# Kernel optimization log

Measured on AMD Instinct MI355X. Metric: run time of the kernel, lower is better.

## Reference

```python
import jax, jax.numpy as jnp
import numpy as np

N = 4096  # number of nodes (matches fill_max of edge indices)


def _dense(edges, n):
    # edges: [2, E] int; dense {0,1} adjacency. Duplicate edges collapse (set semantics).
    return jnp.zeros((n, n), dtype=jnp.float32).at[edges[0], edges[1]].set(1.0)


def setup_inputs() -> dict:
    key = jax.random.key(0)
    ks = jax.random.split(key, 4)
    E = 200000
    mk = lambda k: jax.random.randint(k, (2, E), 0, N, dtype=jnp.int32)
    return {
        "A_pos_t": mk(ks[0]),
        "A_pos_tp1": mk(ks[1]),
        "A_neg_t": mk(ks[2]),
        "A_neg_tp1": mk(ks[3]),
    }


def reference(A_pos_t, A_pos_tp1, A_neg_t, A_neg_tp1):
    p_t = _dense(A_pos_t, N)
    p1 = _dense(A_pos_tp1, N)
    n_t = _dense(A_neg_t, N)
    n1 = _dense(A_neg_tp1, N)

    # edge_index_diff: set symmetric difference == elementwise xor of {0,1} adjacency
    xor_p = p_t + p1 - 2.0 * p_t * p1
    xor_n = n_t + n1 - 2.0 * n_t * n1

    # Balance theory triangle closure on (tp1) graphs.
    # sign(a,b): +1 if pos edge (pos checked first -> priority), -1 elif neg edge.
    sp = p1                      # positive-sign edge indicator
    sn = n1 * (1.0 - p1)         # negative-sign edge indicator (pos has priority)
    off = 1.0 - jnp.eye(N, dtype=jnp.float32)
    spo = sp * off               # exclude b==a / b==c (triples are distinct)
    sno = sn * off

    # number of 2-paths a->b->c with predicted sign +1 / -1
    M_same = spo @ spo + sno @ sno
    M_diff = spo @ sno + sno @ spo

    # the Python loop only infers edges (a,c) with a < c (orientations (i,j,k),(i,k,j),(j,i,k))
    tri = jnp.triu(jnp.ones((N, N), dtype=jnp.float32), k=1)

    ind_p = M_same * tri * (1.0 - p1)  # skip pairs already positively connected
    ind_n = M_diff * tri * (1.0 - n1)  # skip pairs already negatively connected

    # Output: [2, N, N]; entry = xor indicator + indirect-edge multiplicity count
    return jnp.stack([xor_p + ind_p, xor_n + ind_n])
```

## Files before the change

kernel.cpp:

```cpp
#include <hip/hip_runtime.h>


#define NN 4096
#define NW 128
#define MASK_BYTES ((size_t)NN * NW * 4)
#define MASK_WORDS ((size_t)NN * NW)

typedef unsigned int u32;
typedef __attribute__((ext_vector_type(4))) int int4v;
typedef __attribute__((ext_vector_type(4))) float f32x4;

__device__ __forceinline__ void gload_lds16(const char* g, char* l) {
    __builtin_amdgcn_global_load_lds(
        (const __attribute__((address_space(1))) void*)g,
        (__attribute__((address_space(3))) void*)l, 16, 0, 0);
}


__global__ void scatter_all(const int* __restrict__ e0, const int* __restrict__ e1,
                            const int* __restrict__ e2, const int* __restrict__ e3,
                            int E0, int E1, int E2, int E3,
                            u32* __restrict__ ws) {
    int i = blockIdx.x * blockDim.x + threadIdx.x;
    u32* Pt  = ws + 0 * MASK_WORDS;
    u32* P1  = ws + 1 * MASK_WORDS;
    u32* Nt  = ws + 2 * MASK_WORDS;
    u32* N1  = ws + 3 * MASK_WORDS;
    u32* P1T = ws + 4 * MASK_WORDS;
    u32* N1T = ws + 5 * MASK_WORDS;
    if (i < E0) { int r = e0[i], c = e0[i + E0];
        atomicOr(&Pt[r * NW + (c >> 5)], 1u << (c & 31)); }
    if (i < E1) { int r = e1[i], c = e1[i + E1];
        atomicOr(&P1[r * NW + (c >> 5)], 1u << (c & 31));
        atomicOr(&P1T[c * NW + (r >> 5)], 1u << (r & 31)); }
    if (i < E2) { int r = e2[i], c = e2[i + E2];
        atomicOr(&Nt[r * NW + (c >> 5)], 1u << (c & 31)); }
    if (i < E3) { int r = e3[i], c = e3[i + E3];
        atomicOr(&N1[r * NW + (c >> 5)], 1u << (c & 31));
        atomicOr(&N1T[c * NW + (r >> 5)], 1u << (r & 31)); }
}

__device__ __forceinline__ int4v expand_e(u32 sp, u32 sn) {
    int4v E;
    #pragma unroll
    for (int i = 0; i < 4; i++) {
        u32 p = (((sp >> (4 * i)) & 0xFu) * 0x00204081u) & 0x01010101u;
        u32 n = (((sn >> (4 * i)) & 0xFu) * 0x00204081u) & 0x01010101u;
        E[i] = (int)(p | (n << 5));
    }
    return E;
}

__global__ void build_e(const u32* __restrict__ masks,
                        char* __restrict__ E, char* __restrict__ ET) {
    int u = blockIdx.x * blockDim.x + threadIdx.x;
    int half = (u >= (int)MASK_WORDS);
    int wi = half ? u - (int)MASK_WORDS : u;
    const u32* P  = masks + (half ? 4 : 1) * MASK_WORDS;
    const u32* Nm = masks + (half ? 5 : 3) * MASK_WORDS;
    u32 p = P[wi];
    u32 n = Nm[wi] & ~p;
    int a = wi >> 7, col = wi & 127;
    if ((a >> 5) == col) {
        u32 db = 1u << (a & 31);
        p &= ~db; n &= ~db;
    }
    char* dst = (half ? ET : E) + (size_t)a * NN;
    #pragma unroll
    for (int j = 0; j < 2; j++) {
        int kb = col * 32 + j * 16;
        int kbs = (kb & ~127) | (((((kb >> 4) & 7) ^ (a & 7)) & 7) << 4);
        *reinterpret_cast<int4v*>(dst + kbs) =
            expand_e((p >> (16 * j)) & 0xFFFFu, (n >> (16 * j)) & 0xFFFFu);
    }
}

__global__ __launch_bounds__(256, 2) void gemm_ep(
    const char* __restrict__ E, const char* __restrict__ ET,
    const u32* __restrict__ Pt, const u32* __restrict__ P1,
    const u32* __restrict__ Nt, const u32* __restrict__ N1,
    float* __restrict__ out)
{
    const int tid = threadIdx.x;
    const size_t plane = (size_t)NN * NN;

    int s_ = ((int)blockIdx.x & 7) * 66 + ((int)blockIdx.x >> 3);
    int by = (int)((65.0f - sqrtf(4225.0f - 8.0f * (float)s_)) * 0.5f);
    if (by > 31) by = 31;
    while (by > 0 && 32 * by - (by * (by - 1)) / 2 > s_) --by;
    while (32 * (by + 1) - ((by + 1) * by) / 2 <= s_) ++by;
    int bx = by + s_ - (32 * by - (by * (by - 1)) / 2);
    const int a0 = by << 7, c0 = bx << 7;

    __shared__ char EA[2][16384];
    __shared__ char EB[2][16384];

    const int wave = tid >> 6, lane = tid & 63;
    const int wr = (wave >> 1) * 64, wcol = (wave & 1) * 64;
    const int lr = lane & 15, lg = lane >> 4;

    const char* gA = E  + (size_t)(a0 + (tid >> 3)) * NN + (tid & 7) * 16;
    const char* gB = ET + (size_t)(c0 + (tid >> 3)) * NN + (tid & 7) * 16;
    const int wuni = (tid >> 6) * 1024;

    int4v acc[4][4];
    int4v zero = {0, 0, 0, 0};
    #pragma unroll
    for (int m = 0; m < 4; m++)
        #pragma unroll
        for (int n = 0; n < 4; n++) acc[m][n] = zero;

    #pragma unroll
    for (int i = 0; i < 4; i++) {
        gload_lds16(gA + i * 131072, &EA[0][i * 4096 + wuni]);
        gload_lds16(gB + i * 131072, &EB[0][i * 4096 + wuni]);
    }

    if (by != bx) {
        #pragma unroll 4
        for (int pass = 0; pass < 16; ++pass) {
            int e = pass * 1024 + tid * 4;
            int r = e >> 7, cc = e & 127;
            int widx = (c0 + r) * NW + ((a0 + cc) >> 5);
            int sh = cc & 31;
            u32 xp = (P1[widx] ^ Pt[widx]) >> sh;
            u32 xn = (N1[widx] ^ Nt[widx]) >> sh;
            f32x4 o0, o1;
            #pragma unroll
            for (int i = 0; i < 4; i++) {
                o0[i] = (float)((xp >> i) & 1u);
                o1[i] = (float)((xn >> i) & 1u);
            }
            size_t ob = (size_t)(c0 + r) * NN + a0 + cc;
            *reinterpret_cast<f32x4*>(out + ob) = o0;
            *reinterpret_cast<f32x4*>(out + plane + ob) = o1;
        }
    }
    __syncthreads();

    for (int t = 0; t < 32; ++t) {
        const int cur = t & 1;
        if (t < 31) {
            const int off = (t + 1) * 128;
            #pragma unroll
            for (int i = 0; i < 4; i++) {
                gload_lds16(gA + i * 131072 + off, &EA[cur ^ 1][i * 4096 + wuni]);
                gload_lds16(gB + i * 131072 + off, &EB[cur ^ 1][i * 4096 + wuni]);
            }
        }
        #pragma unroll
        for (int ks = 0; ks < 2; ks++) {
            const int kb = ks * 64 + lg * 16;
            int4v ebf[4];
            #pragma unroll
            for (int n = 0; n < 4; n++) {
                int rowb = wcol + n * 16 + lr;
                ebf[n] = *reinterpret_cast<const int4v*>(
                    &EB[cur][rowb * 128 + (kb ^ ((rowb & 7) << 4))]);
            }
            #pragma unroll
            for (int m = 0; m < 4; m++) {
                int rowa = wr + m * 16 + lr;
                int4v eaf = *reinterpret_cast<const int4v*>(
                    &EA[cur][rowa * 128 + (kb ^ ((rowa & 7) << 4))]);
                #pragma unroll
                for (int n = 0; n < 4; n++)
                    acc[m][n] = __builtin_amdgcn_mfma_i32_16x16x64_i8(
                        eaf, ebf[n], acc[m][n], 0, 0, 0);
            }
        }
        __syncthreads();
    }

    #pragma unroll
    for (int m = 0; m < 4; m++) {
        #pragma unroll
        for (int n = 0; n < 4; n++) {
            #pragma unroll
            for (int q = 0; q < 4; q++) {
                int a = a0 + wr + m * 16 + lg * 4 + q;
                int c = c0 + wcol + n * 16 + lr;
                int widx = a * NW + (c >> 5);
                int bit = c & 31;
                u32 p1 = (P1[widx] >> bit) & 1u;
                u32 n1 = (N1[widx] >> bit) & 1u;
                u32 pt = (Pt[widx] >> bit) & 1u;
                u32 nt = (Nt[widx] >> bit) & 1u;
                int av = acc[m][n][q];
                int Ms = (av & 31) + (av >> 10);
                int Md = (av >> 5) & 31;
                int o0 = (int)(pt ^ p1) + ((a < c && !p1) ? Ms : 0);
                int o1 = (int)(nt ^ n1) + ((a < c && !n1) ? Md : 0);
                size_t oi = (size_t)a * NN + c;
                out[oi] = (float)o0;
                out[plane + oi] = (float)o1;
            }
        }
    }
}

extern "C" void kernel_launch(void* const* d_in, const int* in_sizes, int n_in,
                              void* d_out, int out_size, void* d_ws, size_t ws_size,
                              hipStream_t stream) {
    char* ws = (char*)d_ws;
    u32* masks = (u32*)ws;
    u32* Pt = masks + 0 * MASK_WORDS;
    u32* P1 = masks + 1 * MASK_WORDS;
    u32* Nt = masks + 2 * MASK_WORDS;
    u32* N1 = masks + 3 * MASK_WORDS;
    char* E  = ws + 6 * MASK_BYTES;
    char* ET = E + (size_t)NN * NN;

    hipMemsetAsync(d_ws, 0, 6 * MASK_BYTES, stream);

    int E0 = in_sizes[0] / 2, E1 = in_sizes[1] / 2;
    int E2 = in_sizes[2] / 2, E3 = in_sizes[3] / 2;
    int Emax = max(max(E0, E1), max(E2, E3));
    scatter_all<<<(Emax + 255) / 256, 256, 0, stream>>>(
        (const int*)d_in[0], (const int*)d_in[1], (const int*)d_in[2],
        (const int*)d_in[3], E0, E1, E2, E3, masks);

    build_e<<<(2 * (int)MASK_WORDS) / 256, 256, 0, stream>>>(masks, E, ET);

    gemm_ep<<<528, 256, 0, stream>>>(E, ET, Pt, P1, Nt, N1, (float*)d_out);
}
```

Before: 159.2 us.

## Triple-buffer GEMM K-loop with 64-byte slices and defer lower-triangle XOR fill

The pipeline goes from two buffers to three, each holding a 64-wide K slice, and replaces the full __syncthreads with explicit vmcnt waits and a raw barrier, so two loads stay in flight while a stage computes. LDS per block drops from 64KB to 48KB and launch bounds rise to 3 blocks per SM to raise occupancy. build_e now writes unswizzled rows and the swizzle moves to the global source address. The mirrored XOR-only store for off-diagonal tiles moves after the epilogue so it no longer delays the main loop. Possible risks are register pressure under the tighter launch bound and the doubled barrier count.

```diff
diff --git a/kernel.cpp b/kernel.cpp
--- a/kernel.cpp
+++ b/kernel.cpp
@@ -65,17 +65,12 @@
         u32 db = 1u << (a & 31);
         p &= ~db; n &= ~db;
     }
-    char* dst = (half ? ET : E) + (size_t)a * NN;
-    #pragma unroll
-    for (int j = 0; j < 2; j++) {
-        int kb = col * 32 + j * 16;
-        int kbs = (kb & ~127) | (((((kb >> 4) & 7) ^ (a & 7)) & 7) << 4);
-        *reinterpret_cast<int4v*>(dst + kbs) =
-            expand_e((p >> (16 * j)) & 0xFFFFu, (n >> (16 * j)) & 0xFFFFu);
-    }
-}
-
-__global__ __launch_bounds__(256, 2) void gemm_ep(
+    char* dst = (half ? ET : E) + (size_t)a * NN + col * 32;
+    *reinterpret_cast<int4v*>(dst)      = expand_e(p & 0xFFFFu, n & 0xFFFFu);
+    *reinterpret_cast<int4v*>(dst + 16) = expand_e(p >> 16, n >> 16);
+}
+
+__global__ __launch_bounds__(256, 3) void gemm_ep(
     const char* __restrict__ E, const char* __restrict__ ET,
     const u32* __restrict__ Pt, const u32* __restrict__ P1,
     const u32* __restrict__ Nt, const u32* __restrict__ N1,
@@ -92,16 +87,17 @@
     int bx = by + s_ - (32 * by - (by * (by - 1)) / 2);
     const int a0 = by << 7, c0 = bx << 7;
 
-    __shared__ char EA[2][16384];
-    __shared__ char EB[2][16384];
+    __shared__ char LB[3][2][8192];
 
     const int wave = tid >> 6, lane = tid & 63;
     const int wr = (wave >> 1) * 64, wcol = (wave & 1) * 64;
     const int lr = lane & 15, lg = lane >> 4;
 
-    const char* gA = E  + (size_t)(a0 + (tid >> 3)) * NN + (tid & 7) * 16;
-    const char* gB = ET + (size_t)(c0 + (tid >> 3)) * NN + (tid & 7) * 16;
-    const int wuni = (tid >> 6) * 1024;
+    const int rh = tid >> 2, ch = tid & 3;
+    const int swz = (ch ^ ((rh >> 1) & 3)) << 4;
+    const char* gA = E  + (size_t)(a0 + rh) * NN + swz;
+    const char* gB = ET + (size_t)(c0 + rh) * NN + swz;
+    const int l16 = tid * 16;
 
     int4v acc[4][4];
     int4v zero = {0, 0, 0, 0};
@@ -110,67 +106,59 @@
         #pragma unroll
         for (int n = 0; n < 4; n++) acc[m][n] = zero;
 
-    #pragma unroll
-    for (int i = 0; i < 4; i++) {
-        gload_lds16(gA + i * 131072, &EA[0][i * 4096 + wuni]);
-        gload_lds16(gB + i * 131072, &EB[0][i * 4096 + wuni]);
-    }
-
-    if (by != bx) {
-        #pragma unroll 4
-        for (int pass = 0; pass < 16; ++pass) {
-            int e = pass * 1024 + tid * 4;
-            int r = e >> 7, cc = e & 127;
-            int widx = (c0 + r) * NW + ((a0 + cc) >> 5);
-            int sh = cc & 31;
-            u32 xp = (P1[widx] ^ Pt[widx]) >> sh;
-            u32 xn = (N1[widx] ^ Nt[widx]) >> sh;
-            f32x4 o0, o1;
-            #pragma unroll
-            for (int i = 0; i < 4; i++) {
-                o0[i] = (float)((xp >> i) & 1u);
-                o1[i] = (float)((xn >> i) & 1u);
-            }
-            size_t ob = (size_t)(c0 + r) * NN + a0 + cc;
-            *reinterpret_cast<f32x4*>(out + ob) = o0;
-            *reinterpret_cast<f32x4*>(out + plane + ob) = o1;
-        }
-    }
-    __syncthreads();
-
-    for (int t = 0; t < 32; ++t) {
-        const int cur = t & 1;
-        if (t < 31) {
-            const int off = (t + 1) * 128;
-            #pragma unroll
-            for (int i = 0; i < 4; i++) {
-                gload_lds16(gA + i * 131072 + off, &EA[cur ^ 1][i * 4096 + wuni]);
-                gload_lds16(gB + i * 131072 + off, &EB[cur ^ 1][i * 4096 + wuni]);
-            }
-        }
-        #pragma unroll
-        for (int ks = 0; ks < 2; ks++) {
-            const int kb = ks * 64 + lg * 16;
-            int4v ebf[4];
-            #pragma unroll
-            for (int n = 0; n < 4; n++) {
-                int rowb = wcol + n * 16 + lr;
-                ebf[n] = *reinterpret_cast<const int4v*>(
-                    &EB[cur][rowb * 128 + (kb ^ ((rowb & 7) << 4))]);
-            }
-            #pragma unroll
-            for (int m = 0; m < 4; m++) {
-                int rowa = wr + m * 16 + lr;
-                int4v eaf = *reinterpret_cast<const int4v*>(
-                    &EA[cur][rowa * 128 + (kb ^ ((rowa & 7) << 4))]);
-                #pragma unroll
-                for (int n = 0; n < 4; n++)
-                    acc[m][n] = __builtin_amdgcn_mfma_i32_16x16x64_i8(
-                        eaf, ebf[n], acc[m][n], 0, 0, 0);
-            }
-        }
-        __syncthreads();
-    }
+    #define STAGE(b, t)                                               \
+        do {                                                          \
+            const int koff = (t) * 64;                                \
+            gload_lds16(gA + koff,            &LB[b][0][l16]);        \
+            gload_lds16(gA + 64 * NN + koff,  &LB[b][0][4096 + l16]); \
+            gload_lds16(gB + koff,            &LB[b][1][l16]);        \
+            gload_lds16(gB + 64 * NN + koff,  &LB[b][1][4096 + l16]); \
+        } while (0)
+
+    #define COMPUTE(b)                                                         \
+        do {                                                                   \
+            int4v bf[4];                                                       \
+            _Pragma("unroll")                                                  \
+            for (int n = 0; n < 4; n++) {                                      \
+                int rowb = wcol + n * 16 + lr;                                 \
+                bf[n] = *reinterpret_cast<const int4v*>(                       \
+                    &LB[b][1][rowb * 64 + ((lg ^ ((rowb >> 1) & 3)) << 4)]);   \
+            }                                                                  \
+            __builtin_amdgcn_s_setprio(1);                                     \
+            _Pragma("unroll")                                                  \
+            for (int m = 0; m < 4; m++) {                                      \
+                int rowa = wr + m * 16 + lr;                                   \
+                int4v af = *reinterpret_cast<const int4v*>(                    \
+                    &LB[b][0][rowa * 64 + ((lg ^ ((rowa >> 1) & 3)) << 4)]);   \
+                _Pragma("unroll")                                              \
+                for (int n = 0; n < 4; n++)                                    \
+                    acc[m][n] = __builtin_amdgcn_mfma_i32_16x16x64_i8(         \
+                        af, bf[n], acc[m][n], 0, 0, 0);                        \
+            }                                                                  \
+            __builtin_amdgcn_s_setprio(0);                                     \
+        } while (0)
+
+    STAGE(0, 0);
+    STAGE(1, 1);
+    asm volatile("s_waitcnt vmcnt(4)" ::: "memory");
+    __builtin_amdgcn_s_barrier();
+
+    int cur = 0;
+    for (int t = 0; t < 62; ++t) {
+        int nb = cur + 2; if (nb >= 3) nb -= 3;
+        STAGE(nb, t + 2);
+        COMPUTE(cur);
+        asm volatile("s_waitcnt vmcnt(4)" ::: "memory");
+        __builtin_amdgcn_s_barrier();
+        cur = (cur == 2) ? 0 : cur + 1;
+    }
+    COMPUTE(cur);
+    asm volatile("s_waitcnt vmcnt(0)" ::: "memory");
+    __builtin_amdgcn_s_barrier();
+    cur = (cur == 2) ? 0 : cur + 1;
+    COMPUTE(cur);
+    #undef STAGE
+    #undef COMPUTE
 
     #pragma unroll
     for (int m = 0; m < 4; m++) {
@@ -197,6 +185,27 @@
             }
         }
     }
+
+    if (by != bx) {
+        #pragma unroll 4
+        for (int pass = 0; pass < 16; ++pass) {
+            int e = pass * 1024 + tid * 4;
+            int r = e >> 7, cc = e & 127;
+            int widx = (c0 + r) * NW + ((a0 + cc) >> 5);
+            int sh = cc & 31;
+            u32 xp = (P1[widx] ^ Pt[widx]) >> sh;
+            u32 xn = (N1[widx] ^ Nt[widx]) >> sh;
+            f32x4 o0, o1;
+            #pragma unroll
+            for (int i = 0; i < 4; i++) {
+                o0[i] = (float)((xp >> i) & 1u);
+                o1[i] = (float)((xn >> i) & 1u);
+            }
+            size_t ob = (size_t)(c0 + r) * NN + a0 + cc;
+            *reinterpret_cast<f32x4*>(out + ob) = o0;
+            *reinterpret_cast<f32x4*>(out + plane + ob) = o1;
+        }
+    }
 }
 
 extern "C" void kernel_launch(void* const* d_in, const int* in_sizes, int n_in,
```

Result: faster. 150.4 us (-5.5%).

## Transpose masks via ballot, per-wave LDS pipeline, and move xor writes after GEMM

Applied to the files above, without the earlier changes.

The scatter kernel no longer builds transposed P1/N1 masks with extra atomics. The new build kernel makes ET from the untransposed masks using a wave-level ballot transpose, which also shrinks the workspace memset. The GEMM is reorganized so each wave streams its own 64x64 A/B slices into private LDS buffers with a 2-deep global_load_lds prefetch. Waits use explicit vmcnt/lgkmcnt instead of block-wide __syncthreads, and MFMA priority is raised. The mirrored xor-only output writes move after the GEMM epilogue; each wave now loads its own operand data with no sharing, which raises L2 traffic.

```diff
diff --git a/kernel.cpp b/kernel.cpp
--- a/kernel.cpp
+++ b/kernel.cpp
@@ -22,22 +22,18 @@
                             int E0, int E1, int E2, int E3,
                             u32* __restrict__ ws) {
     int i = blockIdx.x * blockDim.x + threadIdx.x;
-    u32* Pt  = ws + 0 * MASK_WORDS;
-    u32* P1  = ws + 1 * MASK_WORDS;
-    u32* Nt  = ws + 2 * MASK_WORDS;
-    u32* N1  = ws + 3 * MASK_WORDS;
-    u32* P1T = ws + 4 * MASK_WORDS;
-    u32* N1T = ws + 5 * MASK_WORDS;
+    u32* Pt = ws + 0 * MASK_WORDS;
+    u32* P1 = ws + 1 * MASK_WORDS;
+    u32* Nt = ws + 2 * MASK_WORDS;
+    u32* N1 = ws + 3 * MASK_WORDS;
     if (i < E0) { int r = e0[i], c = e0[i + E0];
         atomicOr(&Pt[r * NW + (c >> 5)], 1u << (c & 31)); }
     if (i < E1) { int r = e1[i], c = e1[i + E1];
-        atomicOr(&P1[r * NW + (c >> 5)], 1u << (c & 31));
-        atomicOr(&P1T[c * NW + (r >> 5)], 1u << (r & 31)); }
+        atomicOr(&P1[r * NW + (c >> 5)], 1u << (c & 31)); }
     if (i < E2) { int r = e2[i], c = e2[i + E2];
         atomicOr(&Nt[r * NW + (c >> 5)], 1u << (c & 31)); }
     if (i < E3) { int r = e3[i], c = e3[i + E3];
-        atomicOr(&N1[r * NW + (c >> 5)], 1u << (c & 31));
-        atomicOr(&N1T[c * NW + (r >> 5)], 1u << (r & 31)); }
+        atomicOr(&N1[r * NW + (c >> 5)], 1u << (c & 31)); }
 }
 
 __device__ __forceinline__ int4v expand_e(u32 sp, u32 sn) {
@@ -51,27 +47,50 @@
     return E;
 }
 
-__global__ void build_e(const u32* __restrict__ masks,
-                        char* __restrict__ E, char* __restrict__ ET) {
-    int u = blockIdx.x * blockDim.x + threadIdx.x;
-    int half = (u >= (int)MASK_WORDS);
-    int wi = half ? u - (int)MASK_WORDS : u;
-    const u32* P  = masks + (half ? 4 : 1) * MASK_WORDS;
-    const u32* Nm = masks + (half ? 5 : 3) * MASK_WORDS;
-    u32 p = P[wi];
-    u32 n = Nm[wi] & ~p;
-    int a = wi >> 7, col = wi & 127;
-    if ((a >> 5) == col) {
-        u32 db = 1u << (a & 31);
-        p &= ~db; n &= ~db;
-    }
-    char* dst = (half ? ET : E) + (size_t)a * NN;
-    #pragma unroll
-    for (int j = 0; j < 2; j++) {
-        int kb = col * 32 + j * 16;
-        int kbs = (kb & ~127) | (((((kb >> 4) & 7) ^ (a & 7)) & 7) << 4);
-        *reinterpret_cast<int4v*>(dst + kbs) =
-            expand_e((p >> (16 * j)) & 0xFFFFu, (n >> (16 * j)) & 0xFFFFu);
+__global__ void build_both(const u32* __restrict__ masks,
+                           char* __restrict__ E, char* __restrict__ ET) {
+    const u32* P  = masks + 1 * MASK_WORDS;
+    const u32* Nm = masks + 3 * MASK_WORDS;
+    if (blockIdx.x < 2048) {
+        int w = blockIdx.x * 256 + threadIdx.x;
+        u32 p = P[w];
+        u32 n = Nm[w] & ~p;
+        int a = w >> 7, col = w & 127;
+        if ((a >> 5) == col) {
+            u32 db = 1u << (a & 31);
+            p &= ~db; n &= ~db;
+        }
+        char* dst = E + (size_t)a * NN + col * 32;
+        *reinterpret_cast<int4v*>(dst)      = expand_e(p & 0xFFFFu, n & 0xFFFFu);
+        *reinterpret_cast<int4v*>(dst + 16) = expand_e(p >> 16, n >> 16);
+    } else {
+        int gw = (blockIdx.x - 2048) * 4 + (threadIdx.x >> 6);
+        int lane = threadIdx.x & 63;
+        int ab = gw >> 7;
+        int wc = gw & 127;
+        u32 pw = P[(ab * 64 + lane) * NW + wc];
+        u32 nw = Nm[(ab * 64 + lane) * NW + wc];
+        u32 myp = 0, myn = 0;
+        #pragma unroll
+        for (int j = 0; j < 32; j++) {
+            unsigned long long bp = __ballot((pw >> j) & 1u);
+            unsigned long long bn = __ballot((nw >> j) & 1u);
+            if ((lane & 31) == j) {
+                myp = (lane < 32) ? (u32)bp : (u32)(bp >> 32);
+                myn = (lane < 32) ? (u32)bn : (u32)(bn >> 32);
+            }
+        }
+        u32 p = myp;
+        u32 n = myn & ~p;
+        int c = wc * 32 + (lane & 31);
+        int abase = ab * 64 + (lane >> 5) * 32;
+        if (c >= abase && c < abase + 32) {
+            u32 db = 1u << (c - abase);
+            p &= ~db; n &= ~db;
+        }
+        char* dst = ET + (size_t)c * NN + abase;
+        *reinterpret_cast<int4v*>(dst)      = expand_e(p & 0xFFFFu, n & 0xFFFFu);
+        *reinterpret_cast<int4v*>(dst + 16) = expand_e(p >> 16, n >> 16);
     }
 }
 
@@ -92,16 +111,16 @@
     int bx = by + s_ - (32 * by - (by * (by - 1)) / 2);
     const int a0 = by << 7, c0 = bx << 7;
 
-    __shared__ char EA[2][16384];
-    __shared__ char EB[2][16384];
+    __shared__ char LB[4][2][8192];
 
     const int wave = tid >> 6, lane = tid & 63;
     const int wr = (wave >> 1) * 64, wcol = (wave & 1) * 64;
     const int lr = lane & 15, lg = lane >> 4;
-
-    const char* gA = E  + (size_t)(a0 + (tid >> 3)) * NN + (tid & 7) * 16;
-    const char* gB = ET + (size_t)(c0 + (tid >> 3)) * NN + (tid & 7) * 16;
-    const int wuni = (tid >> 6) * 1024;
+    const int ko = (lg ^ ((lr >> 1) & 3)) << 4;
+
+    const int sswz = ((lane & 3) ^ ((lane >> 3) & 3)) << 4;
+    const char* gA = E  + (size_t)(a0 + wr   + (lane >> 2)) * NN + sswz;
+    const char* gB = ET + (size_t)(c0 + wcol + (lane >> 2)) * NN + sswz;
 
     int4v acc[4][4];
     int4v zero = {0, 0, 0, 0};
@@ -110,67 +129,67 @@
         #pragma unroll
         for (int n = 0; n < 4; n++) acc[m][n] = zero;
 
-    #pragma unroll
-    for (int i = 0; i < 4; i++) {
-        gload_lds16(gA + i * 131072, &EA[0][i * 4096 + wuni]);
-        gload_lds16(gB + i * 131072, &EB[0][i * 4096 + wuni]);
-    }
-
-    if (by != bx) {
-        #pragma unroll 4
-        for (int pass = 0; pass < 16; ++pass) {
-            int e = pass * 1024 + tid * 4;
-            int r = e >> 7, cc = e & 127;
-            int widx = (c0 + r) * NW + ((a0 + cc) >> 5);
-            int sh = cc & 31;
-            u32 xp = (P1[widx] ^ Pt[widx]) >> sh;
-            u32 xn = (N1[widx] ^ Nt[widx]) >> sh;
-            f32x4 o0, o1;
-            #pragma unroll
-            for (int i = 0; i < 4; i++) {
-                o0[i] = (float)((xp >> i) & 1u);
-                o1[i] = (float)((xn >> i) & 1u);
-            }
-            size_t ob = (size_t)(c0 + r) * NN + a0 + cc;
-            *reinterpret_cast<f32x4*>(out + ob) = o0;
-            *reinterpret_cast<f32x4*>(out + plane + ob) = o1;
-        }
-    }
-    __syncthreads();
-
-    for (int t = 0; t < 32; ++t) {
+    #define STAGE(b, t)                                                \
+        do {                                                           \
+            const int _kf = (t) * 64;                                  \
+            gload_lds16(gA + _kf,          &LB[wave][b][0]);           \
+            gload_lds16(gA + 65536 + _kf,  &LB[wave][b][1024]);        \
+            gload_lds16(gA + 131072 + _kf, &LB[wave][b][2048]);        \
+            gload_lds16(gA + 196608 + _kf, &LB[wave][b][3072]);        \
+            gload_lds16(gB + _kf,          &LB[wave][b][4096]);        \
+            gload_lds16(gB + 65536 + _kf,  &LB[wave][b][5120]);        \
+            gload_lds16(gB + 131072 + _kf, &LB[wave][b][6144]);        \
+            gload_lds16(gB + 196608 + _kf, &LB[wave][b][7168]);        \
+        } while (0)
+
+    #define FRAGS(b)                                                   \
+        int4v af[4], bf[4];                                            \
+        _Pragma("unroll")                                              \
+        for (int n = 0; n < 4; n++)                                    \
+            bf[n] = *reinterpret_cast<const int4v*>(                   \
+                &LB[wave][b][4096 + (n * 16 + lr) * 64 + ko]);         \
+        _Pragma("unroll")                                              \
+        for (int m = 0; m < 4; m++)                                    \
+            af[m] = *reinterpret_cast<const int4v*>(                   \
+                &LB[wave][b][(m * 16 + lr) * 64 + ko]);
+
+    #define MFMAS()                                                    \
+        __builtin_amdgcn_s_setprio(1);                                 \
+        _Pragma("unroll")                                              \
+        for (int m = 0; m < 4; m++)                                    \
+            _Pragma("unroll")                                          \
+            for (int n = 0; n < 4; n++)                                \
+                acc[m][n] = __builtin_amdgcn_mfma_i32_16x16x64_i8(     \
+                    af[m], bf[n], acc[m][n], 0, 0, 0);                 \
+        __builtin_amdgcn_s_setprio(0);
+
+    STAGE(0, 0);
+    STAGE(1, 1);
+
+    for (int t = 0; t < 62; ++t) {
         const int cur = t & 1;
-        if (t < 31) {
-            const int off = (t + 1) * 128;
-            #pragma unroll
-            for (int i = 0; i < 4; i++) {
-                gload_lds16(gA + i * 131072 + off, &EA[cur ^ 1][i * 4096 + wuni]);
-                gload_lds16(gB + i * 131072 + off, &EB[cur ^ 1][i * 4096 + wuni]);
-            }
-        }
-        #pragma unroll
-        for (int ks = 0; ks < 2; ks++) {
-            const int kb = ks * 64 + lg * 16;
-            int4v ebf[4];
-            #pragma unroll
-            for (int n = 0; n < 4; n++) {
-                int rowb = wcol + n * 16 + lr;
-                ebf[n] = *reinterpret_cast<const int4v*>(
-                    &EB[cur][rowb * 128 + (kb ^ ((rowb & 7) << 4))]);
-            }
-            #pragma unroll
-            for (int m = 0; m < 4; m++) {
-                int rowa = wr + m * 16 + lr;
-                int4v eaf = *reinterpret_cast<const int4v*>(
-                    &EA[cur][rowa * 128 + (kb ^ ((rowa & 7) << 4))]);
-                #pragma unroll
-                for (int n = 0; n < 4; n++)
-                    acc[m][n] = __builtin_amdgcn_mfma_i32_16x16x64_i8(
-                        eaf, ebf[n], acc[m][n], 0, 0, 0);
-            }
-        }
-        __syncthreads();
-    }
+        asm volatile("s_waitcnt vmcnt(8)" ::: "memory");
+        FRAGS(cur);
+        asm volatile("s_waitcnt lgkmcnt(0)" ::: "memory");
+        __builtin_amdgcn_sched_barrier(0);
+        STAGE(cur, t + 2);
+        MFMAS();
+    }
+    {
+        asm volatile("s_waitcnt vmcnt(8)" ::: "memory");
+        FRAGS(0);
+        asm volatile("s_waitcnt lgkmcnt(0)" ::: "memory");
+        MFMAS();
+    }
+    {
+        asm volatile("s_waitcnt vmcnt(0)" ::: "memory");
+        FRAGS(1);
+        asm volatile("s_waitcnt lgkmcnt(0)" ::: "memory");
+        MFMAS();
+    }
+    #undef STAGE
+    #undef FRAGS
+    #undef MFMAS
 
     #pragma unroll
     for (int m = 0; m < 4; m++) {
@@ -197,6 +216,27 @@
             }
         }
     }
+
+    if (by != bx) {
+        #pragma unroll 4
+        for (int pass = 0; pass < 16; ++pass) {
+            int e = pass * 1024 + tid * 4;
+            int r = e >> 7, cc = e & 127;
+            int widx = (c0 + r) * NW + ((a0 + cc) >> 5);
+            int sh = cc & 31;
+            u32 xp = (P1[widx] ^ Pt[widx]) >> sh;
+            u32 xn = (N1[widx] ^ Nt[widx]) >> sh;
+            f32x4 o0, o1;
+            #pragma unroll
+            for (int i = 0; i < 4; i++) {
+                o0[i] = (float)((xp >> i) & 1u);
+                o1[i] = (float)((xn >> i) & 1u);
+            }
+            size_t ob = (size_t)(c0 + r) * NN + a0 + cc;
+            *reinterpret_cast<f32x4*>(out + ob) = o0;
+            *reinterpret_cast<f32x4*>(out + plane + ob) = o1;
+        }
+    }
 }
 
 extern "C" void kernel_launch(void* const* d_in, const int* in_sizes, int n_in,
@@ -208,10 +248,10 @@
     u32* P1 = masks + 1 * MASK_WORDS;
     u32* Nt = masks + 2 * MASK_WORDS;
     u32* N1 = masks + 3 * MASK_WORDS;
-    char* E  = ws + 6 * MASK_BYTES;
+    char* E  = ws + 4 * MASK_BYTES;
     char* ET = E + (size_t)NN * NN;
 
-    hipMemsetAsync(d_ws, 0, 6 * MASK_BYTES, stream);
+    hipMemsetAsync(d_ws, 0, 4 * MASK_BYTES, stream);
 
     int E0 = in_sizes[0] / 2, E1 = in_sizes[1] / 2;
     int E2 = in_sizes[2] / 2, E3 = in_sizes[3] / 2;
@@ -220,7 +260,7 @@
         (const int*)d_in[0], (const int*)d_in[1], (const int*)d_in[2],
         (const int*)d_in[3], E0, E1, E2, E3, masks);
 
-    build_e<<<(2 * (int)MASK_WORDS) / 256, 256, 0, stream>>>(masks, E, ET);
+    build_both<<<4096, 256, 0, stream>>>(masks, E, ET);
 
     gemm_ep<<<528, 256, 0, stream>>>(E, ET, Pt, P1, Nt, N1, (float*)d_out);
 }
```

Result: slower. 164.5 us (+3.3%).
